# Kernel optimization log

Hardware: AMD Instinct MI355X
Metric: run time of the kernel (lower is better)

## Reference

```python
import jax, jax.numpy as jnp
import numpy as np

N = 100000      # nodes
E = 1600000     # edges
IN = 128        # in_channels
H = 128         # hidden_channels
OUT = 40        # out_channels
EPS = 1e-5      # BatchNorm eps


def setup_inputs() -> dict:
    key = jax.random.key(0)
    ks = jax.random.split(key, 16)
    s_in = 1.0 / np.sqrt(IN)
    s_h = 1.0 / np.sqrt(H)
    s_fc = 1.0 / np.sqrt(IN + 2 * H)
    return {
        "x": jax.random.normal(ks[0], (N, IN), dtype=jnp.float32),
        "edge_index": jax.random.randint(ks[1], (2, E), 0, N, dtype=jnp.int32),
        "W1": jax.random.normal(ks[2], (IN, H), dtype=jnp.float32) * s_in,
        "b1": jnp.zeros((H,), dtype=jnp.float32),
        "W2": jax.random.normal(ks[3], (H, H), dtype=jnp.float32) * s_h,
        "b2": jnp.zeros((H,), dtype=jnp.float32),
        "bn1_gamma": jnp.ones((H,), dtype=jnp.float32),
        "bn1_beta": jnp.zeros((H,), dtype=jnp.float32),
        "bn1_mean": jax.random.normal(ks[4], (H,), dtype=jnp.float32) * 0.1,
        "bn1_var": jax.random.uniform(ks[5], (H,), dtype=jnp.float32, minval=0.5, maxval=1.5),
        "bn2_gamma": jnp.ones((H,), dtype=jnp.float32),
        "bn2_beta": jnp.zeros((H,), dtype=jnp.float32),
        "bn2_mean": jax.random.normal(ks[6], (H,), dtype=jnp.float32) * 0.1,
        "bn2_var": jax.random.uniform(ks[7], (H,), dtype=jnp.float32, minval=0.5, maxval=1.5),
        "fc_W": jax.random.normal(ks[8], (IN + 2 * H, OUT), dtype=jnp.float32) * s_fc,
        "fc_b": jnp.zeros((OUT,), dtype=jnp.float32),
    }


def _gcn_conv(x, edge_index, W, b):
    """PyG GCNConv: symmetric norm with self-loops. x:[N,F_in] -> [N,F_out]."""
    row, col = edge_index[0], edge_index[1]  # messages flow col -> row
    h = x @ W                                 # [N, F_out] transform first
    deg = jax.ops.segment_sum(jnp.ones((E,), x.dtype), row, num_segments=N) + 1.0  # +1 self-loop
    dinv = jax.lax.rsqrt(deg)                 # deg^{-1/2}
    norm = dinv[row] * dinv[col]              # [E]
    msg = h[col] * norm[:, None]              # gather + scale
    agg = jax.ops.segment_sum(msg, row, num_segments=N)
    agg = agg + h * (dinv * dinv)[:, None]    # self-loop contribution
    return agg + b


def _bn_eval(x, gamma, beta, mean, var):
    return (x - mean) * (gamma * jax.lax.rsqrt(var + EPS)) + beta


def reference(x, edge_index, W1, b1, W2, b2,
              bn1_gamma, bn1_beta, bn1_mean, bn1_var,
              bn2_gamma, bn2_beta, bn2_mean, bn2_var,
              fc_W, fc_b):
    x0 = x
    x1 = _gcn_conv(x0, edge_index, W1, b1)
    x1 = jax.nn.relu(_bn_eval(x1, bn1_gamma, bn1_beta, bn1_mean, bn1_var))
    # dropout: eval mode -> identity
    x2 = _gcn_conv(x1, edge_index, W2, b2)
    x2 = jax.nn.relu(_bn_eval(x2, bn2_gamma, bn2_beta, bn2_mean, bn2_var))
    out = jnp.concatenate([x0, x1, x2], axis=-1) @ fc_W + fc_b  # [N, OUT]
    return out
```

## Files before the change

kernel.cpp:

```cpp
#include <hip/hip_runtime.h>

#define N_NODES 100000
#define N_EDGES 1600000
#define C_H     128
#define C_OUT   40
#define K_FC    384
#define BN_EPS  1e-5f
#define NB      391
#define CHUNK   6144

typedef unsigned int uint;

__global__ void zero_i32(int* p, int n) {
    int i = blockIdx.x * blockDim.x + threadIdx.x;
    if (i < n) p[i] = 0;
}

__global__ __launch_bounds__(256) void bucket_count(const int* __restrict__ erow,
                                                    int* __restrict__ bcnt) {
    __shared__ int cnt[NB];
    for (int i = threadIdx.x; i < NB; i += 256) cnt[i] = 0;
    __syncthreads();
    const int c0 = blockIdx.x * CHUNK;
    const int c1 = min(c0 + CHUNK, N_EDGES);
    for (int e = c0 + threadIdx.x; e < c1; e += 256)
        atomicAdd(&cnt[erow[e] >> 8], 1);
    __syncthreads();
    for (int i = threadIdx.x; i < NB; i += 256)
        if (cnt[i]) atomicAdd(&bcnt[i], cnt[i]);
}

__global__ __launch_bounds__(256) void scan_buckets(const int* __restrict__ bcnt,
                                                    int* __restrict__ bstart,
                                                    int* __restrict__ bfill) {
    __shared__ int sa[512], sb[512];
    const int t = threadIdx.x;
    int v0 = (t < NB) ? bcnt[t] : 0;
    int v1 = (t + 256 < NB) ? bcnt[t + 256] : 0;
    sa[t] = v0; sa[t + 256] = v1;
    __syncthreads();
    int* src = sa; int* dst = sb;
    for (int off = 1; off < 512; off <<= 1) {
        dst[t]       = src[t]       + (t >= off ? src[t - off] : 0);
        dst[t + 256] = src[t + 256] + (t + 256 >= off ? src[t + 256 - off] : 0);
        __syncthreads();
        int* tmp = src; src = dst; dst = tmp;
    }
    if (t < NB)       { bstart[t] = src[t] - v0;             bfill[t] = src[t] - v0; }
    if (t + 256 < NB) { bstart[t + 256] = src[t + 256] - v1; bfill[t + 256] = src[t + 256] - v1; }
    if (t == 0) bstart[NB] = N_EDGES;
}

__global__ __launch_bounds__(256) void bucket_bin(const int* __restrict__ erow,
                                                  const int* __restrict__ ecol,
                                                  int* __restrict__ bfill,
                                                  int2* __restrict__ pairs) {
    __shared__ int cnt[NB];
    __shared__ int lpos[NB];
    for (int i = threadIdx.x; i < NB; i += 256) cnt[i] = 0;
    __syncthreads();
    const int c0 = blockIdx.x * CHUNK;
    const int c1 = min(c0 + CHUNK, N_EDGES);
    for (int e = c0 + threadIdx.x; e < c1; e += 256)
        atomicAdd(&cnt[erow[e] >> 8], 1);
    __syncthreads();
    for (int i = threadIdx.x; i < NB; i += 256)
        lpos[i] = cnt[i] ? atomicAdd(&bfill[i], cnt[i]) : 0;
    __syncthreads();
    for (int e = c0 + threadIdx.x; e < c1; e += 256) {
        int r = erow[e], c = ecol[e];
        int p = atomicAdd(&lpos[r >> 8], 1);
        pairs[p] = make_int2(r, c);
    }
}

__global__ __launch_bounds__(256) void bucket_csr(const int2* __restrict__ pairs,
                                                  const int* __restrict__ bstart,
                                                  int* __restrict__ rowptr,
                                                  float* __restrict__ dinv,
                                                  int* __restrict__ colsg) {
    __shared__ int lcnt[256], sa[256], sb[256], lpos[256];
    const int b = blockIdx.x;
    const int t = threadIdx.x;
    const int p0 = bstart[b], p1 = bstart[b + 1];
    lcnt[t] = 0;
    __syncthreads();
    for (int i = p0 + t; i < p1; i += 256)
        atomicAdd(&lcnt[pairs[i].x & 255], 1);
    __syncthreads();
    sa[t] = lcnt[t];
    __syncthreads();
    int* src = sa; int* dst = sb;
    for (int off = 1; off < 256; off <<= 1) {
        dst[t] = src[t] + (t >= off ? src[t - off] : 0);
        __syncthreads();
        int* tmp = src; src = dst; dst = tmp;
    }
    const int excl = src[t] - lcnt[t];
    const int r = b * 256 + t;
    if (r < N_NODES) {
        rowptr[r] = p0 + excl;
        dinv[r] = rsqrtf((float)lcnt[t] + 1.0f);
    }
    if (b == NB - 1 && t == 0) rowptr[N_NODES] = N_EDGES;
    lpos[t] = excl;
    __syncthreads();
    for (int i = p0 + t; i < p1; i += 256) {
        int2 pr = pairs[i];
        int s = atomicAdd(&lpos[pr.x & 255], 1);
        colsg[p0 + s] = pr.y;
    }
}

__global__ void bn_coef(const float* b1, const float* g1, const float* be1,
                        const float* m1, const float* v1,
                        const float* b2, const float* g2, const float* be2,
                        const float* m2, const float* v2,
                        float* s1, float* t1, float* s2, float* t2) {
    int f = threadIdx.x;
    float sa = g1[f] * rsqrtf(v1[f] + BN_EPS);
    s1[f] = sa;
    t1[f] = (b1[f] - m1[f]) * sa + be1[f];
    float sb = g2[f] * rsqrtf(v2[f] + BN_EPS);
    s2[f] = sb;
    t2[f] = (b2[f] - m2[f]) * sb + be2[f];
}

#define FMA4(A, S, V) \
    A.x = fmaf(S, V.x, A.x); A.y = fmaf(S, V.y, A.y); \
    A.z = fmaf(S, V.z, A.z); A.w = fmaf(S, V.w, A.w);

__device__ inline uint pack_bf16x2(float a, float b) {
    uint ua = __builtin_bit_cast(uint, a);
    uint ub = __builtin_bit_cast(uint, b);
    ua += 0x7fffu + ((ua >> 16) & 1u);
    ub += 0x7fffu + ((ub >> 16) & 1u);
    return (ua >> 16) | (ub & 0xffff0000u);
}

__global__ __launch_bounds__(256) void gemm_scaled(const float* __restrict__ X,
                                                   const float* __restrict__ W,
                                                   const float* __restrict__ dinv,
                                                   uint* __restrict__ Hs) {
    __shared__ float wl[64 * 128];
    __shared__ float xl[32 * 68];

    const int tid = threadIdx.x;
    const int rg = tid >> 5;
    const int c4 = (tid & 31) << 2;
    const int rb = blockIdx.x * 32;
    const int r0 = rb + rg * 4;

    float4 acc0 = {0,0,0,0}, acc1 = {0,0,0,0}, acc2 = {0,0,0,0}, acc3 = {0,0,0,0};

    for (int half = 0; half < 2; ++half) {
        const int k0 = half * 64;
        __syncthreads();
        {
            const float4* W4 = (const float4*)(W + (size_t)k0 * 128);
            float4* wl4 = (float4*)wl;
            #pragma unroll
            for (int i = 0; i < 8; ++i) wl4[tid + i * 256] = W4[tid + i * 256];
        }
        #pragma unroll
        for (int i = 0; i < 2; ++i) {
            int f = tid + i * 256;
            int row = f >> 4, cc = f & 15;
            float4 v = *(const float4*)(X + (size_t)(rb + row) * 128 + k0 + cc * 4);
            *(float4*)&xl[row * 68 + cc * 4] = v;
        }
        __syncthreads();

        for (int k4 = 0; k4 < 16; ++k4) {
            const float* wr = wl + k4 * 4 * 128 + c4;
            float4 w0 = *(const float4*)(wr);
            float4 w1 = *(const float4*)(wr + 128);
            float4 w2 = *(const float4*)(wr + 256);
            float4 w3 = *(const float4*)(wr + 384);
            float4 xv0 = *(const float4*)&xl[(rg * 4 + 0) * 68 + k4 * 4];
            float4 xv1 = *(const float4*)&xl[(rg * 4 + 1) * 68 + k4 * 4];
            float4 xv2 = *(const float4*)&xl[(rg * 4 + 2) * 68 + k4 * 4];
            float4 xv3 = *(const float4*)&xl[(rg * 4 + 3) * 68 + k4 * 4];
            FMA4(acc0, xv0.x, w0) FMA4(acc0, xv0.y, w1) FMA4(acc0, xv0.z, w2) FMA4(acc0, xv0.w, w3)
            FMA4(acc1, xv1.x, w0) FMA4(acc1, xv1.y, w1) FMA4(acc1, xv1.z, w2) FMA4(acc1, xv1.w, w3)
            FMA4(acc2, xv2.x, w0) FMA4(acc2, xv2.y, w1) FMA4(acc2, xv2.z, w2) FMA4(acc2, xv2.w, w3)
            FMA4(acc3, xv3.x, w0) FMA4(acc3, xv3.y, w1) FMA4(acc3, xv3.z, w2) FMA4(acc3, xv3.w, w3)
        }
    }
    float d0 = dinv[r0], d1 = dinv[r0 + 1], d2 = dinv[r0 + 2], d3 = dinv[r0 + 3];
    uint2 o;
    o.x = pack_bf16x2(acc0.x * d0, acc0.y * d0);
    o.y = pack_bf16x2(acc0.z * d0, acc0.w * d0);
    *(uint2*)(Hs + (size_t)(r0 + 0) * 64 + (c4 >> 1)) = o;
    o.x = pack_bf16x2(acc1.x * d1, acc1.y * d1);
    o.y = pack_bf16x2(acc1.z * d1, acc1.w * d1);
    *(uint2*)(Hs + (size_t)(r0 + 1) * 64 + (c4 >> 1)) = o;
    o.x = pack_bf16x2(acc2.x * d2, acc2.y * d2);
    o.y = pack_bf16x2(acc2.z * d2, acc2.w * d2);
    *(uint2*)(Hs + (size_t)(r0 + 2) * 64 + (c4 >> 1)) = o;
    o.x = pack_bf16x2(acc3.x * d3, acc3.y * d3);
    o.y = pack_bf16x2(acc3.z * d3, acc3.w * d3);
    *(uint2*)(Hs + (size_t)(r0 + 3) * 64 + (c4 >> 1)) = o;
}

#define ACC1(V) \
    accx += __builtin_bit_cast(float, V << 16); \
    accy += __builtin_bit_cast(float, V & 0xffff0000u);

__global__ __launch_bounds__(256) void spmm_bn_relu4(
    const uint* __restrict__ Hs, const int* __restrict__ cols,
    const int* __restrict__ rowptr, const float* __restrict__ dinv,
    const float* __restrict__ s, const float* __restrict__ t,
    float* __restrict__ Y) {
    const int lane = threadIdx.x & 63;
    const int r = blockIdx.x * 4 + (threadIdx.x >> 6);

    uint vself = Hs[(size_t)r * 64 + lane];
    float accx = __builtin_bit_cast(float, vself << 16);
    float accy = __builtin_bit_cast(float, vself & 0xffff0000u);
    const float di = dinv[r];
    const int e0 = rowptr[r], e1 = rowptr[r + 1];
    int j = e0;
    const int n16 = e0 + ((e1 - e0) & ~15);
    for (; j < n16; j += 16) {
        uint v[16];
        #pragma unroll
        for (int q = 0; q < 16; ++q)
            v[q] = Hs[(size_t)cols[j + q] * 64 + lane];
        #pragma unroll
        for (int q = 0; q < 16; ++q) { ACC1(v[q]) }
    }
    const int n4 = e0 + ((e1 - e0) & ~3);
    for (; j < n4; j += 4) {
        uint v[4];
        #pragma unroll
        for (int q = 0; q < 4; ++q)
            v[q] = Hs[(size_t)cols[j + q] * 64 + lane];
        #pragma unroll
        for (int q = 0; q < 4; ++q) { ACC1(v[q]) }
    }
    for (; j < e1; ++j) {
        uint v0 = Hs[(size_t)cols[j] * 64 + lane];
        ACC1(v0)
    }
    float2 sf = ((const float2*)s)[lane];
    float2 tf = ((const float2*)t)[lane];
    float2 o;
    o.x = fmaxf(fmaf(accx * di, sf.x, tf.x), 0.0f);
    o.y = fmaxf(fmaf(accy * di, sf.y, tf.y), 0.0f);
    ((float2*)Y)[(size_t)r * 64 + lane] = o;
}

__global__ __launch_bounds__(256) void final_gemm11(
    const float* __restrict__ X0, const float* __restrict__ X1,
    const float* __restrict__ X2, const float* __restrict__ fcW,
    const float* __restrict__ fcb, float* __restrict__ out) {
    const int t = threadIdx.x;
    const int lane = t & 63;
    const int wq = __builtin_amdgcn_readfirstlane(t >> 6);
    const int r = blockIdx.x * 64 + lane;
    if (r >= N_NODES) return;

    float acc[10];
    #pragma unroll
    for (int c = 0; c < 10; ++c) acc[c] = 0.0f;

    const float* segs[3] = {X0, X1, X2};
    #pragma unroll
    for (int seg = 0; seg < 3; ++seg) {
        const float4* xrow = (const float4*)(segs[seg] + (size_t)r * 128);
        const float* wseg = fcW + (size_t)seg * 128 * 40 + wq * 10;
        #pragma unroll 2
        for (int k4 = 0; k4 < 32; ++k4) {
            float4 xv = xrow[k4];
            const float* w0 = wseg + (size_t)k4 * 160;
            #pragma unroll
            for (int c = 0; c < 10; ++c) {
                acc[c] = fmaf(xv.x, w0[c],        acc[c]);
                acc[c] = fmaf(xv.y, w0[40 + c],   acc[c]);
                acc[c] = fmaf(xv.z, w0[80 + c],   acc[c]);
                acc[c] = fmaf(xv.w, w0[120 + c],  acc[c]);
            }
        }
    }

    #pragma unroll
    for (int c2 = 0; c2 < 5; ++c2) {
        float2 o;
        o.x = acc[c2 * 2 + 0] + fcb[wq * 10 + c2 * 2 + 0];
        o.y = acc[c2 * 2 + 1] + fcb[wq * 10 + c2 * 2 + 1];
        *(float2*)(out + (size_t)r * 40 + wq * 10 + c2 * 2) = o;
    }
}

extern "C" void kernel_launch(void* const* d_in, const int* in_sizes, int n_in,
                              void* d_out, int out_size, void* d_ws, size_t ws_size,
                              hipStream_t stream) {
    const float* x   = (const float*)d_in[0];
    const int*   ei  = (const int*)d_in[1];
    const int* e_row = ei;
    const int* e_col = ei + N_EDGES;
    const float* W1  = (const float*)d_in[2];
    const float* b1  = (const float*)d_in[3];
    const float* W2  = (const float*)d_in[4];
    const float* b2  = (const float*)d_in[5];
    const float* g1  = (const float*)d_in[6];
    const float* be1 = (const float*)d_in[7];
    const float* m1  = (const float*)d_in[8];
    const float* v1  = (const float*)d_in[9];
    const float* g2  = (const float*)d_in[10];
    const float* be2 = (const float*)d_in[11];
    const float* m2  = (const float*)d_in[12];
    const float* v2  = (const float*)d_in[13];
    const float* fcW = (const float*)d_in[14];
    const float* fcb = (const float*)d_in[15];
    float* out = (float*)d_out;

    char* ws = (char*)d_ws;
    size_t off = 0;
    auto alloc = [&](size_t b) {
        char* p = ws + off;
        off += (b + 255) & ~(size_t)255;
        return p;
    };
    uint*  h      = (uint*)alloc((size_t)N_NODES * C_H * 2);
    float* x1     = (float*)alloc((size_t)N_NODES * C_H * 4);
    float* x2     = (float*)alloc((size_t)N_NODES * C_H * 4);
    int2*  pairs  = (int2*)alloc((size_t)N_EDGES * 8);
    int*   cols   = (int*)alloc((size_t)N_EDGES * 4);
    float* dinv   = (float*)alloc(N_NODES * 4);
    int*   rowptr = (int*)alloc((N_NODES + 1) * 4);
    int*   bcnt   = (int*)alloc((NB + 1) * 4);
    int*   bstart = (int*)alloc((NB + 1) * 4);
    int*   bfill  = (int*)alloc((NB + 1) * 4);
    float* coef   = (float*)alloc(512 * 4);
    float* s1 = coef, *t1 = coef + 128, *s2 = coef + 256, *t2 = coef + 384;

    const int nwg_bin = (N_EDGES + CHUNK - 1) / CHUNK;

    zero_i32<<<2, 256, 0, stream>>>(bcnt, NB);
    bucket_count<<<nwg_bin, 256, 0, stream>>>(e_row, bcnt);
    scan_buckets<<<1, 256, 0, stream>>>(bcnt, bstart, bfill);
    bucket_bin<<<nwg_bin, 256, 0, stream>>>(e_row, e_col, bfill, pairs);
    bucket_csr<<<NB, 256, 0, stream>>>(pairs, bstart, rowptr, dinv, cols);
    bn_coef<<<1, 128, 0, stream>>>(b1, g1, be1, m1, v1, b2, g2, be2, m2, v2,
                                   s1, t1, s2, t2);

    gemm_scaled<<<N_NODES / 32, 256, 0, stream>>>(x, W1, dinv, h);
    spmm_bn_relu4<<<N_NODES / 4, 256, 0, stream>>>(h, cols, rowptr, dinv, s1, t1, x1);
    gemm_scaled<<<N_NODES / 32, 256, 0, stream>>>(x1, W2, dinv, h);
    spmm_bn_relu4<<<N_NODES / 4, 256, 0, stream>>>(h, cols, rowptr, dinv, s2, t2, x2);
    final_gemm11<<<(N_NODES + 63) / 64, 256, 0, stream>>>(x, x1, x2, fcW, fcb, out);
}
```

Before: 505.2 us.

## Stage final FC input rows through double-buffered LDS with coalesced loads

Rewrites the final concat-GEMM so each wavefront cooperatively loads 16-column chunks of 64 rows with coalesced float4 loads into a padded, double-buffered LDS tile, prefetching the next chunk while computing the current one. The old kernel had each lane read its own row with strided float4 loads. The mapping also changes: each block now covers 256 rows for one of four 10-column output groups, with the column group taken from the block index, where before the four waves of a block split the columns of the same 64 rows. Rows are now fetched by four different blocks rather than shared within one block, so this relies on L2 reuse and adds LDS traffic and register pressure.

```diff
diff --git a/kernel.cpp b/kernel.cpp
--- a/kernel.cpp
+++ b/kernel.cpp
@@ -251,45 +251,81 @@
     ((float2*)Y)[(size_t)r * 64 + lane] = o;
 }
 
-__global__ __launch_bounds__(256) void final_gemm11(
+__global__ __launch_bounds__(256) void final_gemm12(
     const float* __restrict__ X0, const float* __restrict__ X1,
     const float* __restrict__ X2, const float* __restrict__ fcW,
     const float* __restrict__ fcb, float* __restrict__ out) {
+    __shared__ float xs[4 * 2 * 64 * 20];
+
     const int t = threadIdx.x;
     const int lane = t & 63;
-    const int wq = __builtin_amdgcn_readfirstlane(t >> 6);
-    const int r = blockIdx.x * 64 + lane;
-    if (r >= N_NODES) return;
+    const int wid = t >> 6;
+    const int cg = blockIdx.x & 3;
+    const int rb = (blockIdx.x >> 2) * 256 + wid * 64;
+    const float* wbase = fcW + cg * 10;
+    float* xw = xs + wid * 2560;
 
     float acc[10];
     #pragma unroll
     for (int c = 0; c < 10; ++c) acc[c] = 0.0f;
 
-    const float* segs[3] = {X0, X1, X2};
-    #pragma unroll
-    for (int seg = 0; seg < 3; ++seg) {
-        const float4* xrow = (const float4*)(segs[seg] + (size_t)r * 128);
-        const float* wseg = fcW + (size_t)seg * 128 * 40 + wq * 10;
-        #pragma unroll 2
-        for (int k4 = 0; k4 < 32; ++k4) {
-            float4 xv = xrow[k4];
-            const float* w0 = wseg + (size_t)k4 * 160;
+    const int sr = lane >> 2;
+    const int qk = lane & 3;
+    float4 g0, g1, g2, g3;
+
+    auto issue = [&](int ch) {
+        const float* xseg = (ch < 8) ? X0 : (ch < 16) ? X1 : X2;
+        const int koff = (ch & 7) * 16 + qk * 4;
+        int r0 = rb + 0 * 16 + sr, r1 = rb + 1 * 16 + sr;
+        int r2 = rb + 2 * 16 + sr, r3 = rb + 3 * 16 + sr;
+        float4 z = {0, 0, 0, 0};
+        g0 = (r0 < N_NODES) ? *(const float4*)(xseg + (size_t)r0 * 128 + koff) : z;
+        g1 = (r1 < N_NODES) ? *(const float4*)(xseg + (size_t)r1 * 128 + koff) : z;
+        g2 = (r2 < N_NODES) ? *(const float4*)(xseg + (size_t)r2 * 128 + koff) : z;
+        g3 = (r3 < N_NODES) ? *(const float4*)(xseg + (size_t)r3 * 128 + koff) : z;
+    };
+    auto store = [&](int buf) {
+        float* b = xw + buf * 1280;
+        *(float4*)(b + (0 * 16 + sr) * 20 + qk * 4) = g0;
+        *(float4*)(b + (1 * 16 + sr) * 20 + qk * 4) = g1;
+        *(float4*)(b + (2 * 16 + sr) * 20 + qk * 4) = g2;
+        *(float4*)(b + (3 * 16 + sr) * 20 + qk * 4) = g3;
+    };
+
+    issue(0);
+    store(0);
+    issue(1);
+
+    #pragma unroll 2
+    for (int ch = 0; ch < 24; ++ch) {
+        const float* row = xw + (ch & 1) * 1280 + lane * 20;
+        const int kbase = ch * 16;
+        #pragma unroll
+        for (int j = 0; j < 4; ++j) {
+            float4 xv = *(const float4*)(row + j * 4);
             #pragma unroll
-            for (int c = 0; c < 10; ++c) {
-                acc[c] = fmaf(xv.x, w0[c],        acc[c]);
-                acc[c] = fmaf(xv.y, w0[40 + c],   acc[c]);
-                acc[c] = fmaf(xv.z, w0[80 + c],   acc[c]);
-                acc[c] = fmaf(xv.w, w0[120 + c],  acc[c]);
+            for (int e = 0; e < 4; ++e) {
+                const float* wk = wbase + (size_t)(kbase + j * 4 + e) * 40;
+                float xve = (e == 0) ? xv.x : (e == 1) ? xv.y
+                          : (e == 2) ? xv.z : xv.w;
+                #pragma unroll
+                for (int c = 0; c < 10; ++c)
+                    acc[c] = fmaf(xve, wk[c], acc[c]);
             }
         }
-    }
-
-    #pragma unroll
-    for (int c2 = 0; c2 < 5; ++c2) {
-        float2 o;
-        o.x = acc[c2 * 2 + 0] + fcb[wq * 10 + c2 * 2 + 0];
-        o.y = acc[c2 * 2 + 1] + fcb[wq * 10 + c2 * 2 + 1];
-        *(float2*)(out + (size_t)r * 40 + wq * 10 + c2 * 2) = o;
+        if (ch < 23) store((ch + 1) & 1);
+        if (ch < 22) issue(ch + 2);
+    }
+
+    const int r = rb + lane;
+    if (r < N_NODES) {
+        #pragma unroll
+        for (int c2 = 0; c2 < 5; ++c2) {
+            float2 o;
+            o.x = acc[c2 * 2 + 0] + fcb[cg * 10 + c2 * 2 + 0];
+            o.y = acc[c2 * 2 + 1] + fcb[cg * 10 + c2 * 2 + 1];
+            *(float2*)(out + (size_t)r * 40 + cg * 10 + c2 * 2) = o;
+        }
     }
 }
 
@@ -350,5 +386,5 @@
     spmm_bn_relu4<<<N_NODES / 4, 256, 0, stream>>>(h, cols, rowptr, dinv, s1, t1, x1);
     gemm_scaled<<<N_NODES / 32, 256, 0, stream>>>(x1, W2, dinv, h);
     spmm_bn_relu4<<<N_NODES / 4, 256, 0, stream>>>(h, cols, rowptr, dinv, s2, t2, x2);
-    final_gemm11<<<(N_NODES + 63) / 64, 256, 0, stream>>>(x, x1, x2, fcW, fcb, out);
-}
+    final_gemm12<<<((N_NODES + 255) / 256) * 4, 256, 0, stream>>>(x, x1, x2, fcW, fcb, out);
+}
```

Measured after the change: 732.9 us. 1.45x slower.

## Split final GEMM reduction dimension across waves with LDS reduction

Applied to the files above, without the earlier changes.

The final fully connected kernel now assigns each wave a quarter of the 384-long reduction dimension instead of a quarter of the output columns. Each row of the concatenated input is therefore read once per block rather than once per wave. Partial sums for all 40 outputs are reduced through shared memory, and the output is written with coalesced stores. The cost is 40 accumulator registers, about 41KB of LDS per block and a block barrier, which may limit occupancy.

```diff
diff --git a/kernel.cpp b/kernel.cpp
--- a/kernel.cpp
+++ b/kernel.cpp
@@ -251,45 +251,59 @@
     ((float2*)Y)[(size_t)r * 64 + lane] = o;
 }
 
-__global__ __launch_bounds__(256) void final_gemm11(
+__global__ __launch_bounds__(256) void final_gemm17(
     const float* __restrict__ X0, const float* __restrict__ X1,
     const float* __restrict__ X2, const float* __restrict__ fcW,
     const float* __restrict__ fcb, float* __restrict__ out) {
+    __shared__ float red[4 * 64 * 41];
+
     const int t = threadIdx.x;
     const int lane = t & 63;
-    const int wq = __builtin_amdgcn_readfirstlane(t >> 6);
-    const int r = blockIdx.x * 64 + lane;
-    if (r >= N_NODES) return;
-
-    float acc[10];
+    const int wid = __builtin_amdgcn_readfirstlane(t >> 6);
+    const int rb = blockIdx.x * 64;
+    const int r = rb + lane;
+    const bool valid = r < N_NODES;
+
+    float acc[40];
     #pragma unroll
-    for (int c = 0; c < 10; ++c) acc[c] = 0.0f;
-
-    const float* segs[3] = {X0, X1, X2};
+    for (int c = 0; c < 40; ++c) acc[c] = 0.0f;
+
+    const float* xr0 = X0 + (size_t)r * 128;
+    const float* xr1 = X1 + (size_t)r * 128;
+    const float* xr2 = X2 + (size_t)r * 128;
+
+    for (int j = 0; j < 24; ++j) {
+        const int c = wid * 24 + j;
+        const float* xr = (c < 32) ? xr0 : (c < 64) ? xr1 : xr2;
+        const int coff = c & 31;
+        float4 xv = {0, 0, 0, 0};
+        if (valid) xv = *(const float4*)(xr + coff * 4);
+        const float* wk = fcW + (size_t)c * 160;
+        #pragma unroll
+        for (int e = 0; e < 4; ++e) {
+            float xe = (e == 0) ? xv.x : (e == 1) ? xv.y
+                     : (e == 2) ? xv.z : xv.w;
+            #pragma unroll
+            for (int cc = 0; cc < 40; ++cc)
+                acc[cc] = fmaf(xe, wk[e * 40 + cc], acc[cc]);
+        }
+    }
+
+    float* myred = red + (wid * 64 + lane) * 41;
     #pragma unroll
-    for (int seg = 0; seg < 3; ++seg) {
-        const float4* xrow = (const float4*)(segs[seg] + (size_t)r * 128);
-        const float* wseg = fcW + (size_t)seg * 128 * 40 + wq * 10;
-        #pragma unroll 2
-        for (int k4 = 0; k4 < 32; ++k4) {
-            float4 xv = xrow[k4];
-            const float* w0 = wseg + (size_t)k4 * 160;
-            #pragma unroll
-            for (int c = 0; c < 10; ++c) {
-                acc[c] = fmaf(xv.x, w0[c],        acc[c]);
-                acc[c] = fmaf(xv.y, w0[40 + c],   acc[c]);
-                acc[c] = fmaf(xv.z, w0[80 + c],   acc[c]);
-                acc[c] = fmaf(xv.w, w0[120 + c],  acc[c]);
-            }
-        }
-    }
+    for (int cc = 0; cc < 40; ++cc) myred[cc] = acc[cc];
+    __syncthreads();
 
     #pragma unroll
-    for (int c2 = 0; c2 < 5; ++c2) {
-        float2 o;
-        o.x = acc[c2 * 2 + 0] + fcb[wq * 10 + c2 * 2 + 0];
-        o.y = acc[c2 * 2 + 1] + fcb[wq * 10 + c2 * 2 + 1];
-        *(float2*)(out + (size_t)r * 40 + wq * 10 + c2 * 2) = o;
+    for (int i = 0; i < 10; ++i) {
+        int o = i * 256 + t;
+        int row = o / 40, col = o - row * 40;
+        float s = red[(0 * 64 + row) * 41 + col]
+                + red[(1 * 64 + row) * 41 + col]
+                + red[(2 * 64 + row) * 41 + col]
+                + red[(3 * 64 + row) * 41 + col] + fcb[col];
+        int gr = rb + row;
+        if (gr < N_NODES) out[(size_t)gr * 40 + col] = s;
     }
 }
 
@@ -350,5 +364,5 @@
     spmm_bn_relu4<<<N_NODES / 4, 256, 0, stream>>>(h, cols, rowptr, dinv, s1, t1, x1);
     gemm_scaled<<<N_NODES / 32, 256, 0, stream>>>(x1, W2, dinv, h);
     spmm_bn_relu4<<<N_NODES / 4, 256, 0, stream>>>(h, cols, rowptr, dinv, s2, t2, x2);
-    final_gemm11<<<(N_NODES + 63) / 64, 256, 0, stream>>>(x, x1, x2, fcW, fcb, out);
-}
+    final_gemm17<<<(N_NODES + 63) / 64, 256, 0, stream>>>(x, x1, x2, fcW, fcb, out);
+}
```

New measurement: 539.3 us. 1.07x slower.
